# Optimization experiments

Hardware: AMD Instinct MI355X
Metric: run time of the kernel (lower is better)

## Reference

```python
import jax, jax.numpy as jnp
import numpy as np

N_REC_STEPS = 50      # fixed-point iterations for geodesic reconstruction
BN_EPS = 1e-3         # keras BatchNormalization default epsilon


def _dilation2d(x, k):
    # tf.nn.dilation2d, SAME padding: out[p,q] = max_{i,j} x[p+i-1,q+j-1] + k[i,j]
    kk = k[:, :, 0, 0]
    H, W = x.shape[1], x.shape[2]
    xp = jnp.pad(x, ((0, 0), (1, 1), (1, 1), (0, 0)), constant_values=-np.inf)
    vals = [xp[:, i:i + H, j:j + W, :] + kk[i, j] for i in range(3) for j in range(3)]
    return jnp.max(jnp.stack(vals, axis=0), axis=0)


def _erosion2d(x, k):
    # tf.nn.erosion2d (kernel mirrored): out[p,q] = min_{i,j} x[p+i-1,q+j-1] - k[-i,-j]
    kk = k[::-1, ::-1, 0, 0]
    H, W = x.shape[1], x.shape[2]
    xp = jnp.pad(x, ((0, 0), (1, 1), (1, 1), (0, 0)), constant_values=np.inf)
    vals = [xp[:, i:i + H, j:j + W, :] - kk[i, j] for i in range(3) for j in range(3)]
    return jnp.min(jnp.stack(vals, axis=0), axis=0)


def _conv_relu(x, w, b):
    y = jax.lax.conv_general_dilated(x, w, (1, 1), 'VALID',
                                     dimension_numbers=('NHWC', 'HWIO', 'NHWC'))
    return jax.nn.relu(y + b)


def _bn(x, g, b, m, v):
    return g * (x - m) * jax.lax.rsqrt(v + BN_EPS) + b


def _maxpool2(x):
    return jax.lax.reduce_window(x, -np.inf, jax.lax.max,
                                 (1, 2, 2, 1), (1, 2, 2, 1), 'VALID')


def _dilate3_same(x):
    # flat 3x3 structuring element (skimage square(3)) geodesic dilation step
    return jax.lax.reduce_window(x, -np.inf, jax.lax.max,
                                 (1, 3, 3, 1), (1, 1, 1, 1), 'SAME')


def _h_maxima(h, mask):
    # reconstruction-by-dilation of (mask - h) under mask
    marker = mask - h
    def step(m, _):
        m = jnp.minimum(_dilate3_same(m), mask)
        return m, None
    rec, _ = jax.lax.scan(step, marker, None, length=N_REC_STEPS)
    return rec


def setup_inputs() -> dict:
    key = jax.random.key(0)
    ks = jax.random.split(key, 8)
    B, H, W = 32, 256, 256
    inp = {
        'x': jax.random.uniform(ks[0], (B, H, W, 1), dtype=jnp.float32),
        'kernel_open': jnp.zeros((3, 3, 1, 1), jnp.float32),   # flat SE (zero-init)
        'kernel_close': jnp.zeros((3, 3, 1, 1), jnp.float32),
        'conv1_w': 0.1 * jax.random.normal(ks[1], (3, 3, 1, 8), jnp.float32),
        'conv1_b': jnp.zeros((8,), jnp.float32),
        'conv2_w': 0.1 * jax.random.normal(ks[2], (3, 3, 8, 16), jnp.float32),
        'conv2_b': jnp.zeros((16,), jnp.float32),
        'conv3_w': 0.1 * jax.random.normal(ks[3], (3, 3, 16, 32), jnp.float32),
        'conv3_b': jnp.zeros((32,), jnp.float32),
        'conv4_w': 0.1 * jax.random.normal(ks[4], (3, 3, 32, 32), jnp.float32),
        'conv4_b': jnp.zeros((32,), jnp.float32),
        'bn1_g': jnp.ones((8,), jnp.float32), 'bn1_b': jnp.zeros((8,), jnp.float32),
        'bn1_m': jnp.zeros((8,), jnp.float32), 'bn1_v': jnp.ones((8,), jnp.float32),
        'bn2_g': jnp.ones((16,), jnp.float32), 'bn2_b': jnp.zeros((16,), jnp.float32),
        'bn2_m': jnp.zeros((16,), jnp.float32), 'bn2_v': jnp.ones((16,), jnp.float32),
        'bn3_g': jnp.ones((32,), jnp.float32), 'bn3_b': jnp.zeros((32,), jnp.float32),
        'bn3_m': jnp.zeros((32,), jnp.float32), 'bn3_v': jnp.ones((32,), jnp.float32),
        'dense_w': 0.05 * jax.random.uniform(ks[5], (32, 1), dtype=jnp.float32),  # NonNeg
        'dense_b': jnp.zeros((1,), jnp.float32),
    }
    return inp


def reference(x, kernel_open, kernel_close,
              conv1_w, conv1_b, conv2_w, conv2_b, conv3_w, conv3_b, conv4_w, conv4_b,
              bn1_g, bn1_b, bn1_m, bn1_v,
              bn2_g, bn2_b, bn2_m, bn2_v,
              bn3_g, bn3_b, bn3_m, bn3_v,
              dense_w, dense_b):
    # Opening2D then Closing2D (morphological pre-filter)
    xo = _dilation2d(_erosion2d(x, kernel_open), kernel_open)
    xc = _erosion2d(_dilation2d(xo, kernel_close), kernel_close)
    y = _conv_relu(xc, conv1_w, conv1_b)                 # (B,254,254,8)
    y = _bn(y, bn1_g, bn1_b, bn1_m, bn1_v)
    y = _conv_relu(y, conv2_w, conv2_b)                  # (B,252,252,16)
    y = _maxpool2(y)                                     # (B,126,126,16)
    y = _bn(y, bn2_g, bn2_b, bn2_m, bn2_v)
    y = _conv_relu(y, conv3_w, conv3_b)                  # (B,124,124,32)
    y = _bn(y, bn3_g, bn3_b, bn3_m, bn3_v)
    y = _conv_relu(y, conv4_w, conv4_b)                  # (B,122,122,32)
    y = _maxpool2(y)                                     # (B,61,61,32)
    y = jnp.max(y, axis=(1, 2))                          # GlobalMaxPooling2D -> (B,32)
    h = y @ dense_w + dense_b                            # (B,1)
    h = h[:, :, None, None]                              # (B,1,1,1)
    # h-maxima transform: reconstruction by dilation of (xc - h) under xc
    out = _h_maxima(h, xc)                               # (B,256,256,1)
    return (out, h)
```

## Files before the change

kernel.cpp:

```cpp
#include <hip/hip_runtime.h>


#define B_ 32
#define H_ 256
#define W_ 256

__device__ __forceinline__ float4 ld4(const float* p){ return *reinterpret_cast<const float4*>(p); }
__device__ __forceinline__ void st4(float* p, float4 v){ *reinterpret_cast<float4*>(p) = v; }
__device__ __forceinline__ void st4s(float* p, float4 v){ *reinterpret_cast<float4*>(p) = v; }

template<int IS_MAX>
__global__ void morph_k(const float* __restrict__ in, float* __restrict__ out,
                        const float* __restrict__ k9)
{
    int t = blockIdx.x * blockDim.x + threadIdx.x;
    int xq = t & 63; int y = (t >> 6) & 255; int b = t >> 14;
    if (b >= B_) return;
    const float INF = __builtin_inff();
    const float* img = in + (size_t)b * (H_ * W_);
    int x0 = xq * 4;
    float res[4];
    #pragma unroll
    for (int j = 0; j < 4; ++j) res[j] = IS_MAX ? -INF : INF;
    #pragma unroll
    for (int di = -1; di <= 1; ++di) {
        int yy = y + di;
        if (yy < 0 || yy >= H_) continue;
        const float* row = img + yy * W_;
        float w[6];
        w[0] = (x0 > 0) ? row[x0 - 1] : (IS_MAX ? -INF : INF);
        float4 m = ld4(row + x0);
        w[1] = m.x; w[2] = m.y; w[3] = m.z; w[4] = m.w;
        w[5] = (x0 + 4 < W_) ? row[x0 + 4] : (IS_MAX ? -INF : INF);
        #pragma unroll
        for (int dj = -1; dj <= 1; ++dj) {
            float kv = IS_MAX ? k9[(di + 1) * 3 + (dj + 1)]
                              : k9[(1 - di) * 3 + (1 - dj)];
            #pragma unroll
            for (int j = 0; j < 4; ++j) {
                float v = IS_MAX ? (w[j + 1 + dj] + kv) : (w[j + 1 + dj] - kv);
                res[j] = IS_MAX ? fmaxf(res[j], v) : fminf(res[j], v);
            }
        }
    }
    st4(out + (size_t)b * (H_ * W_) + y * W_ + x0,
        make_float4(res[0], res[1], res[2], res[3]));
}

__global__ void conv1_k(const float* __restrict__ xc, float* __restrict__ y1,
                        const float* __restrict__ w, const float* __restrict__ bias,
                        const float* __restrict__ g, const float* __restrict__ bb,
                        const float* __restrict__ mn, const float* __restrict__ vr)
{
    const int S = 254;
    int t = blockIdx.x * blockDim.x + threadIdx.x;
    int total = B_ * S * S;
    if (t >= total) return;
    int x = t % S; int y = (t / S) % S; int b = t / (S * S);
    const float* img = xc + (size_t)b * H_ * W_;
    float acc[8];
    #pragma unroll
    for (int c = 0; c < 8; ++c) acc[c] = bias[c];
    #pragma unroll
    for (int ky = 0; ky < 3; ++ky) {
        #pragma unroll
        for (int kx = 0; kx < 3; ++kx) {
            float iv = img[(y + ky) * W_ + (x + kx)];
            const float* wp = w + (ky * 3 + kx) * 8;
            #pragma unroll
            for (int c = 0; c < 8; ++c) acc[c] = fmaf(iv, wp[c], acc[c]);
        }
    }
    float* op = y1 + (size_t)t * 8;
    #pragma unroll
    for (int c = 0; c < 8; ++c) {
        float z = fmaxf(acc[c], 0.f);
        float s = g[c] / sqrtf(vr[c] + 1.0e-3f);
        op[c] = fmaf(s, z, bb[c] - mn[c] * s);
    }
}

__global__ void conv2_k(const float* __restrict__ y1, float* __restrict__ y2,
                        const float* __restrict__ w, const float* __restrict__ bias,
                        const float* __restrict__ g, const float* __restrict__ bb,
                        const float* __restrict__ mn, const float* __restrict__ vr)
{
    const int P = 126, SIN = 254;
    int t = blockIdx.x * blockDim.x + threadIdx.x;
    int total = B_ * P * P;
    if (t >= total) return;
    int px = t % P; int py = (t / P) % P; int b = t / (P * P);
    const float* imgb = y1 + (size_t)b * SIN * SIN * 8;
    float best[16];
    #pragma unroll
    for (int c = 0; c < 16; ++c) best[c] = 0.f;
    #pragma unroll 1
    for (int pos = 0; pos < 4; ++pos) {
        int oy = 2 * py + (pos >> 1), ox = 2 * px + (pos & 1);
        float acc[16];
        #pragma unroll
        for (int c = 0; c < 16; ++c) acc[c] = bias[c];
        #pragma unroll 1
        for (int tap = 0; tap < 9; ++tap) {
            int ky = tap / 3, kx = tap - ky * 3;
            const float* ip = imgb + ((size_t)(oy + ky) * SIN + (ox + kx)) * 8;
            float4 a = ld4(ip), c4 = ld4(ip + 4);
            float in8[8] = {a.x, a.y, a.z, a.w, c4.x, c4.y, c4.z, c4.w};
            const float* wp = w + tap * 8 * 16;
            #pragma unroll
            for (int ci = 0; ci < 8; ++ci)
                #pragma unroll
                for (int co = 0; co < 16; ++co)
                    acc[co] = fmaf(in8[ci], wp[ci * 16 + co], acc[co]);
        }
        #pragma unroll
        for (int co = 0; co < 16; ++co)
            best[co] = fmaxf(best[co], fmaxf(acc[co], 0.f));
    }
    float* op = y2 + (size_t)t * 16;
    #pragma unroll
    for (int c = 0; c < 16; ++c) {
        float s = g[c] / sqrtf(vr[c] + 1.0e-3f);
        op[c] = fmaf(s, best[c], bb[c] - mn[c] * s);
    }
}

template<int CIN, int CIN_P, int SIN>
__device__ __forceinline__ void conv_tile_compute(
    const float* __restrict__ in_b, const float* __restrict__ w,
    const float* __restrict__ bias, float* lds,
    int ty, int tx, int lty, int ltx, int tid, float acc[32])
{
    const int CINq = CIN / 4;
    const int TOT = 18 * 18 * CINq;
    int y0 = ty * 16, x0 = tx * 16;
    for (int i = tid; i < TOT; i += 256) {
        int pix = i / CINq, q = i - pix * CINq;
        int r = pix / 18, c = pix - r * 18;
        int gy = min(y0 + r, SIN - 1), gx = min(x0 + c, SIN - 1);
        float4 v = ld4(in_b + ((size_t)gy * SIN + gx) * CIN + q * 4);
        st4s(lds + (r * 18 + c) * CIN_P + q * 4, v);
    }
    __syncthreads();
    #pragma unroll
    for (int c = 0; c < 32; ++c) acc[c] = bias[c];
    const float* wt = w;
    #pragma unroll 1
    for (int tap = 0; tap < 9; ++tap) {
        int ky = tap / 3, kx = tap - ky * 3;
        const float* lp = lds + ((lty + ky) * 18 + (ltx + kx)) * CIN_P;
        float v[CIN];
        #pragma unroll
        for (int q = 0; q < CINq; ++q) {
            float4 t4 = *reinterpret_cast<const float4*>(lp + q * 4);
            v[q * 4 + 0] = t4.x; v[q * 4 + 1] = t4.y;
            v[q * 4 + 2] = t4.z; v[q * 4 + 3] = t4.w;
        }
        #pragma unroll
        for (int ci = 0; ci < CIN; ++ci)
            #pragma unroll
            for (int co = 0; co < 32; ++co)
                acc[co] = fmaf(v[ci], wt[ci * 32 + co], acc[co]);
        wt += CIN * 32;
    }
}

__global__ void __launch_bounds__(256) conv3t_k(
    const float* __restrict__ y2, float* __restrict__ y3,
    const float* __restrict__ w, const float* __restrict__ bias,
    const float* __restrict__ g, const float* __restrict__ bb,
    const float* __restrict__ mn, const float* __restrict__ vr)
{
    const int SIN = 126, SOUT = 124;
    __shared__ float lds[18 * 18 * 20];
    int blk = blockIdx.x;
    int b = blk >> 6; int tt = blk & 63; int ty = tt >> 3, tx = tt & 7;
    int tid = threadIdx.x, lty = tid >> 4, ltx = tid & 15;
    float acc[32];
    conv_tile_compute<16, 20, 126>(y2 + (size_t)b * SIN * SIN * 16, w, bias,
                                   lds, ty, tx, lty, ltx, tid, acc);
    int oy = ty * 16 + lty, ox = tx * 16 + ltx;
    if (oy < SOUT && ox < SOUT) {
        float* op = y3 + ((size_t)b * SOUT * SOUT + (size_t)oy * SOUT + ox) * 32;
        #pragma unroll
        for (int c = 0; c < 32; ++c) {
            float z = fmaxf(acc[c], 0.f);
            float s = g[c] / sqrtf(vr[c] + 1.0e-3f);
            op[c] = fmaf(s, z, bb[c] - mn[c] * s);
        }
    }
}

__global__ void __launch_bounds__(256) conv4t_k(
    const float* __restrict__ y3, float* __restrict__ maxbuf,
    const float* __restrict__ w, const float* __restrict__ bias)
{
    const int SIN = 124, SOUT = 122;
    __shared__ float lds[18 * 18 * 36];
    __shared__ float red[4 * 32];
    int blk = blockIdx.x;
    int b = blk >> 6; int tt = blk & 63; int ty = tt >> 3, tx = tt & 7;
    int tid = threadIdx.x, lty = tid >> 4, ltx = tid & 15;
    float acc[32];
    conv_tile_compute<32, 36, 124>(y3 + (size_t)b * SIN * SIN * 32, w, bias,
                                   lds, ty, tx, lty, ltx, tid, acc);
    int oy = ty * 16 + lty, ox = tx * 16 + ltx;
    bool valid = (oy < SOUT) && (ox < SOUT);
    #pragma unroll
    for (int c = 0; c < 32; ++c)
        acc[c] = valid ? fmaxf(acc[c], 0.f) : 0.f;
    int lane = tid & 63, wid = tid >> 6;
    #pragma unroll 1
    for (int c = 0; c < 32; ++c) {
        float v = acc[c];
        #pragma unroll
        for (int off = 32; off >= 1; off >>= 1)
            v = fmaxf(v, __shfl_xor(v, off, 64));
        if (lane == 0) red[wid * 32 + c] = v;
    }
    __syncthreads();
    if (tid < 32) {
        int c = tid;
        float mx = fmaxf(fmaxf(red[0 * 32 + c], red[1 * 32 + c]),
                         fmaxf(red[2 * 32 + c], red[3 * 32 + c]));
        atomicMax(reinterpret_cast<int*>(maxbuf) + b * 32 + c, __float_as_int(mx));
    }
}

__global__ void dense_k(const float* __restrict__ maxbuf, const float* __restrict__ dw,
                        const float* __restrict__ db, float* __restrict__ hbuf,
                        float* __restrict__ out_h)
{
    int t = threadIdx.x;
    if (t < B_) {
        float acc = db[0];
        #pragma unroll
        for (int c = 0; c < 32; ++c) acc = fmaf(maxbuf[t * 32 + c], dw[c], acc);
        hbuf[t] = acc;
        out_h[t] = acc;
    }
}

__global__ void minit_k(const float* __restrict__ xc, const float* __restrict__ hbuf,
                        float* __restrict__ m0)
{
    int t = blockIdx.x * blockDim.x + threadIdx.x;
    int b = t >> 14;
    if (b >= B_) return;
    float hv = hbuf[b];
    float4 a = ld4(xc + (size_t)t * 4);
    st4(m0 + (size_t)t * 4, make_float4(a.x - hv, a.y - hv, a.z - hv, a.w - hv));
}

#define FS_R   5
#define FS_IW  80
#define FS_IH  42
__global__ void __launch_bounds__(256) fstep_k(
    const float* __restrict__ msrc, const float* __restrict__ mask,
    float* __restrict__ mdst)
{
    __shared__ float bufA[FS_IH * FS_IW];
    __shared__ float bufB[FS_IH * FS_IW];
    __shared__ float mk[FS_IH * FS_IW];
    const float NINF = -__builtin_inff();

    int blk = blockIdx.x;
    int img = blk >> 5; int tt = blk & 31; int ty = tt >> 2, tx = tt & 3;
    int gy0 = ty * 32 - FS_R;
    int gx0 = tx * 64 - 8;
    int tid = threadIdx.x;
    const float* src_b = msrc + (size_t)img * (H_ * W_);
    const float* msk_b = mask + (size_t)img * (H_ * W_);

    for (int i = tid; i < FS_IH * FS_IW; i += 256) {
        int r = i / FS_IW, c = i - r * FS_IW;
        int gy = gy0 + r, gx = gx0 + c;
        bool in = (gy >= 0) && (gy < H_) && (gx >= 0) && (gx < W_);
        int gidx = gy * W_ + gx;
        bufA[i] = in ? src_b[gidx] : NINF;
        mk[i]   = in ? msk_b[gidx] : NINF;
    }
    __syncthreads();

    float* cur = bufA;
    float* nxt = bufB;
    #pragma unroll 1
    for (int s = 0; s < FS_R; ++s) {
        for (int i = tid; i < FS_IH * (FS_IW / 4); i += 256) {
            int r = i / (FS_IW / 4), q = i - r * (FS_IW / 4);
            int c = q * 4;
            int rm = (r > 0) ? r - 1 : 0, rp = (r < FS_IH - 1) ? r + 1 : FS_IH - 1;
            float h0, h1, h2, h3;
            {
                const float* rw = cur + rm * FS_IW;
                float4 a = *reinterpret_cast<const float4*>(rw + c);
                float L = rw[(c > 0) ? c - 1 : 0];
                float R = rw[(c + 4 < FS_IW) ? c + 4 : FS_IW - 1];
                h0 = fmaxf(fmaxf(L, a.x), a.y);
                h1 = fmaxf(fmaxf(a.x, a.y), a.z);
                h2 = fmaxf(fmaxf(a.y, a.z), a.w);
                h3 = fmaxf(fmaxf(a.z, a.w), R);
            }
            {
                const float* rw = cur + r * FS_IW;
                float4 a = *reinterpret_cast<const float4*>(rw + c);
                float L = rw[(c > 0) ? c - 1 : 0];
                float R = rw[(c + 4 < FS_IW) ? c + 4 : FS_IW - 1];
                h0 = fmaxf(h0, fmaxf(fmaxf(L, a.x), a.y));
                h1 = fmaxf(h1, fmaxf(fmaxf(a.x, a.y), a.z));
                h2 = fmaxf(h2, fmaxf(fmaxf(a.y, a.z), a.w));
                h3 = fmaxf(h3, fmaxf(fmaxf(a.z, a.w), R));
            }
            {
                const float* rw = cur + rp * FS_IW;
                float4 a = *reinterpret_cast<const float4*>(rw + c);
                float L = rw[(c > 0) ? c - 1 : 0];
                float R = rw[(c + 4 < FS_IW) ? c + 4 : FS_IW - 1];
                h0 = fmaxf(h0, fmaxf(fmaxf(L, a.x), a.y));
                h1 = fmaxf(h1, fmaxf(fmaxf(a.x, a.y), a.z));
                h2 = fmaxf(h2, fmaxf(fmaxf(a.y, a.z), a.w));
                h3 = fmaxf(h3, fmaxf(fmaxf(a.z, a.w), R));
            }
            float4 m4 = *reinterpret_cast<const float4*>(mk + r * FS_IW + c);
            float4 o;
            o.x = fminf(h0, m4.x); o.y = fminf(h1, m4.y);
            o.z = fminf(h2, m4.z); o.w = fminf(h3, m4.w);
            *reinterpret_cast<float4*>(nxt + r * FS_IW + c) = o;
        }
        __syncthreads();
        float* tmp = cur; cur = nxt; nxt = tmp;
    }

    float* dst_b = mdst + (size_t)img * (H_ * W_);
    for (int i = tid; i < 32 * 16; i += 256) {
        int r = i >> 4, q = i & 15;
        float4 v = *reinterpret_cast<const float4*>(cur + (FS_R + r) * FS_IW + 8 + q * 4);
        *reinterpret_cast<float4*>(dst_b + (ty * 32 + r) * W_ + tx * 64 + q * 4) = v;
    }
}

extern "C" void kernel_launch(void* const* d_in, const int* in_sizes, int n_in,
                              void* d_out, int out_size, void* d_ws, size_t ws_size,
                              hipStream_t stream) {
    const float* x    = (const float*)d_in[0];
    const float* ko   = (const float*)d_in[1];
    const float* kc   = (const float*)d_in[2];
    const float* c1w  = (const float*)d_in[3];
    const float* c1b  = (const float*)d_in[4];
    const float* c2w  = (const float*)d_in[5];
    const float* c2b  = (const float*)d_in[6];
    const float* c3w  = (const float*)d_in[7];
    const float* c3b  = (const float*)d_in[8];
    const float* c4w  = (const float*)d_in[9];
    const float* c4b  = (const float*)d_in[10];
    const float* bn1g = (const float*)d_in[11];
    const float* bn1b = (const float*)d_in[12];
    const float* bn1m = (const float*)d_in[13];
    const float* bn1v = (const float*)d_in[14];
    const float* bn2g = (const float*)d_in[15];
    const float* bn2b = (const float*)d_in[16];
    const float* bn2m = (const float*)d_in[17];
    const float* bn2v = (const float*)d_in[18];
    const float* bn3g = (const float*)d_in[19];
    const float* bn3b = (const float*)d_in[20];
    const float* bn3m = (const float*)d_in[21];
    const float* bn3v = (const float*)d_in[22];
    const float* dw   = (const float*)d_in[23];
    const float* db   = (const float*)d_in[24];
    float* out = (float*)d_out;
    float* ws  = (float*)d_ws;

    float* xc     = ws;
    float* A      = ws + 2097152;
    float* Bbuf   = ws + 18613248;
    float* maxbuf = ws + 26741760;
    float* hbuf   = ws + 26742784;
    float* t0 = A;
    float* t1 = A + 2097152;

    const int NQ_BLOCKS = (B_ * H_ * W_ / 4) / 256;

    morph_k<0><<<NQ_BLOCKS, 256, 0, stream>>>(x,  t0, ko);
    morph_k<1><<<NQ_BLOCKS, 256, 0, stream>>>(t0, t1, ko);
    morph_k<1><<<NQ_BLOCKS, 256, 0, stream>>>(t1, t0, kc);
    morph_k<0><<<NQ_BLOCKS, 256, 0, stream>>>(t0, xc, kc);

    conv1_k<<<(B_ * 254 * 254 + 255) / 256, 256, 0, stream>>>(xc, A, c1w, c1b,
                                                              bn1g, bn1b, bn1m, bn1v);
    conv2_k<<<(B_ * 126 * 126 + 255) / 256, 256, 0, stream>>>(A, Bbuf, c2w, c2b,
                                                              bn2g, bn2b, bn2m, bn2v);
    conv3t_k<<<B_ * 64, 256, 0, stream>>>(Bbuf, A, c3w, c3b, bn3g, bn3b, bn3m, bn3v);
    hipMemsetAsync(maxbuf, 0, 32 * 32 * sizeof(float), stream);
    conv4t_k<<<B_ * 64, 256, 0, stream>>>(A, maxbuf, c4w, c4b);
    dense_k<<<1, 64, 0, stream>>>(maxbuf, dw, db, hbuf, out + B_ * H_ * W_);

    minit_k<<<NQ_BLOCKS, 256, 0, stream>>>(xc, hbuf, t0);
    for (int j = 0; j < 10; ++j) {
        const float* src = (j & 1) ? t1 : t0;
        float* dst = (j == 9) ? out : ((j & 1) ? t0 : t1);
        fstep_k<<<B_ * 32, 256, 0, stream>>>(src, xc, dst);
    }
}
```

Measured before the change: 674.0 us.

## Tile conv2 through LDS and chunk conv4 input channels to cut LDS use

Conv2+maxpool becomes a tiled kernel. Each block stages a 34x34x8 input patch in shared memory in channel-planar layout and computes four conv outputs per thread before pooling, replacing uncoalesced per-thread global loads. Conv4 now loads its 32 input channels in two 16-channel chunks, shrinking its shared tile from 36 to 20 floats per pixel so more blocks can be resident per CU. The cost is an extra barrier and reload pass in conv4, and a larger per-thread register accumulator (64 floats) in conv2.

```diff
diff --git a/kernel.cpp b/kernel.cpp
--- a/kernel.cpp
+++ b/kernel.cpp
@@ -80,88 +80,112 @@
     }
 }
 
-__global__ void conv2_k(const float* __restrict__ y1, float* __restrict__ y2,
-                        const float* __restrict__ w, const float* __restrict__ bias,
-                        const float* __restrict__ g, const float* __restrict__ bb,
-                        const float* __restrict__ mn, const float* __restrict__ vr)
-{
-    const int P = 126, SIN = 254;
-    int t = blockIdx.x * blockDim.x + threadIdx.x;
-    int total = B_ * P * P;
-    if (t >= total) return;
-    int px = t % P; int py = (t / P) % P; int b = t / (P * P);
-    const float* imgb = y1 + (size_t)b * SIN * SIN * 8;
-    float best[16];
-    #pragma unroll
-    for (int c = 0; c < 16; ++c) best[c] = 0.f;
+#define C2_PITCH (34 * 34 + 2)
+__global__ void __launch_bounds__(256) conv2t_k(
+    const float* __restrict__ y1, float* __restrict__ y2,
+    const float* __restrict__ w, const float* __restrict__ bias,
+    const float* __restrict__ g, const float* __restrict__ bb,
+    const float* __restrict__ mn, const float* __restrict__ vr)
+{
+    const int SIN = 254, POUT = 126;
+    __shared__ float lds[8 * C2_PITCH];
+    int blk = blockIdx.x;
+    int b = blk >> 6; int tt = blk & 63; int ty = tt >> 3, tx = tt & 7;
+    int cy0 = ty * 32, cx0 = tx * 32;
+    int tid = threadIdx.x;
+    const float* in_b = y1 + (size_t)b * SIN * SIN * 8;
+
+    for (int i = tid; i < 34 * 34; i += 256) {
+        int r = i / 34, c = i - r * 34;
+        int gy = min(cy0 + r, SIN - 1), gx = min(cx0 + c, SIN - 1);
+        const float* p = in_b + ((size_t)gy * SIN + gx) * 8;
+        float4 a = ld4(p), d = ld4(p + 4);
+        lds[0 * C2_PITCH + i] = a.x; lds[1 * C2_PITCH + i] = a.y;
+        lds[2 * C2_PITCH + i] = a.z; lds[3 * C2_PITCH + i] = a.w;
+        lds[4 * C2_PITCH + i] = d.x; lds[5 * C2_PITCH + i] = d.y;
+        lds[6 * C2_PITCH + i] = d.z; lds[7 * C2_PITCH + i] = d.w;
+    }
+    __syncthreads();
+
+    int lty = tid >> 4, ltx = tid & 15;
+    float acc[4][16];
+    #pragma unroll
+    for (int pos = 0; pos < 4; ++pos)
+        #pragma unroll
+        for (int c = 0; c < 16; ++c) acc[pos][c] = bias[c];
+
     #pragma unroll 1
-    for (int pos = 0; pos < 4; ++pos) {
-        int oy = 2 * py + (pos >> 1), ox = 2 * px + (pos & 1);
-        float acc[16];
-        #pragma unroll
-        for (int c = 0; c < 16; ++c) acc[c] = bias[c];
+    for (int tap = 0; tap < 9; ++tap) {
+        int ky = tap / 3, kx = tap - ky * 3;
+        const float* wp = w + tap * 8 * 16;
+        #pragma unroll
+        for (int pos = 0; pos < 4; ++pos) {
+            int pix = (2 * lty + (pos >> 1) + ky) * 34 + (2 * ltx + (pos & 1) + kx);
+            float in8[8];
+            #pragma unroll
+            for (int ci = 0; ci < 8; ++ci) in8[ci] = lds[ci * C2_PITCH + pix];
+            #pragma unroll
+            for (int ci = 0; ci < 8; ++ci)
+                #pragma unroll
+                for (int co = 0; co < 16; ++co)
+                    acc[pos][co] = fmaf(in8[ci], wp[ci * 16 + co], acc[pos][co]);
+        }
+    }
+
+    int py = ty * 16 + lty, px = tx * 16 + ltx;
+    if (py < POUT && px < POUT) {
+        float* op = y2 + ((size_t)b * POUT * POUT + (size_t)py * POUT + px) * 16;
+        #pragma unroll
+        for (int co = 0; co < 16; ++co) {
+            float bst = fmaxf(fmaxf(fmaxf(acc[0][co], 0.f), fmaxf(acc[1][co], 0.f)),
+                              fmaxf(fmaxf(acc[2][co], 0.f), fmaxf(acc[3][co], 0.f)));
+            float s = g[co] / sqrtf(vr[co] + 1.0e-3f);
+            op[co] = fmaf(s, bst, bb[co] - mn[co] * s);
+        }
+    }
+}
+
+template<int CIN, int NCH, int CHP, int SIN>
+__device__ __forceinline__ void conv_tile_chunked(
+    const float* __restrict__ in_b, const float* __restrict__ w,
+    const float* __restrict__ bias, float* lds,
+    int y0, int x0, int lty, int ltx, int tid, float acc[32])
+{
+    const int CHUNK = CIN / NCH, CHQ = CHUNK / 4;
+    #pragma unroll
+    for (int c = 0; c < 32; ++c) acc[c] = bias[c];
+    #pragma unroll 1
+    for (int ch = 0; ch < NCH; ++ch) {
+        int ci0 = ch * CHUNK;
+        if (ch) __syncthreads();
+        const int TOT = 18 * 18 * CHQ;
+        for (int i = tid; i < TOT; i += 256) {
+            int pix = i / CHQ, q = i - pix * CHQ;
+            int r = pix / 18, c = pix - r * 18;
+            int gy = min(y0 + r, SIN - 1), gx = min(x0 + c, SIN - 1);
+            float4 v = ld4(in_b + ((size_t)gy * SIN + gx) * CIN + ci0 + q * 4);
+            st4s(lds + (r * 18 + c) * CHP + q * 4, v);
+        }
+        __syncthreads();
+        const float* wb = w + ci0 * 32;
         #pragma unroll 1
         for (int tap = 0; tap < 9; ++tap) {
             int ky = tap / 3, kx = tap - ky * 3;
-            const float* ip = imgb + ((size_t)(oy + ky) * SIN + (ox + kx)) * 8;
-            float4 a = ld4(ip), c4 = ld4(ip + 4);
-            float in8[8] = {a.x, a.y, a.z, a.w, c4.x, c4.y, c4.z, c4.w};
-            const float* wp = w + tap * 8 * 16;
-            #pragma unroll
-            for (int ci = 0; ci < 8; ++ci)
+            const float* lp = lds + ((lty + ky) * 18 + (ltx + kx)) * CHP;
+            float v[CHUNK];
+            #pragma unroll
+            for (int q = 0; q < CHQ; ++q) {
+                float4 t4 = *reinterpret_cast<const float4*>(lp + q * 4);
+                v[q * 4 + 0] = t4.x; v[q * 4 + 1] = t4.y;
+                v[q * 4 + 2] = t4.z; v[q * 4 + 3] = t4.w;
+            }
+            const float* wt = wb + tap * CIN * 32;
+            #pragma unroll
+            for (int ci = 0; ci < CHUNK; ++ci)
                 #pragma unroll
-                for (int co = 0; co < 16; ++co)
-                    acc[co] = fmaf(in8[ci], wp[ci * 16 + co], acc[co]);
-        }
-        #pragma unroll
-        for (int co = 0; co < 16; ++co)
-            best[co] = fmaxf(best[co], fmaxf(acc[co], 0.f));
-    }
-    float* op = y2 + (size_t)t * 16;
-    #pragma unroll
-    for (int c = 0; c < 16; ++c) {
-        float s = g[c] / sqrtf(vr[c] + 1.0e-3f);
-        op[c] = fmaf(s, best[c], bb[c] - mn[c] * s);
-    }
-}
-
-template<int CIN, int CIN_P, int SIN>
-__device__ __forceinline__ void conv_tile_compute(
-    const float* __restrict__ in_b, const float* __restrict__ w,
-    const float* __restrict__ bias, float* lds,
-    int ty, int tx, int lty, int ltx, int tid, float acc[32])
-{
-    const int CINq = CIN / 4;
-    const int TOT = 18 * 18 * CINq;
-    int y0 = ty * 16, x0 = tx * 16;
-    for (int i = tid; i < TOT; i += 256) {
-        int pix = i / CINq, q = i - pix * CINq;
-        int r = pix / 18, c = pix - r * 18;
-        int gy = min(y0 + r, SIN - 1), gx = min(x0 + c, SIN - 1);
-        float4 v = ld4(in_b + ((size_t)gy * SIN + gx) * CIN + q * 4);
-        st4s(lds + (r * 18 + c) * CIN_P + q * 4, v);
-    }
-    __syncthreads();
-    #pragma unroll
-    for (int c = 0; c < 32; ++c) acc[c] = bias[c];
-    const float* wt = w;
-    #pragma unroll 1
-    for (int tap = 0; tap < 9; ++tap) {
-        int ky = tap / 3, kx = tap - ky * 3;
-        const float* lp = lds + ((lty + ky) * 18 + (ltx + kx)) * CIN_P;
-        float v[CIN];
-        #pragma unroll
-        for (int q = 0; q < CINq; ++q) {
-            float4 t4 = *reinterpret_cast<const float4*>(lp + q * 4);
-            v[q * 4 + 0] = t4.x; v[q * 4 + 1] = t4.y;
-            v[q * 4 + 2] = t4.z; v[q * 4 + 3] = t4.w;
-        }
-        #pragma unroll
-        for (int ci = 0; ci < CIN; ++ci)
-            #pragma unroll
-            for (int co = 0; co < 32; ++co)
-                acc[co] = fmaf(v[ci], wt[ci * 32 + co], acc[co]);
-        wt += CIN * 32;
+                for (int co = 0; co < 32; ++co)
+                    acc[co] = fmaf(v[ci], wt[ci * 32 + co], acc[co]);
+        }
     }
 }
 
@@ -177,8 +201,8 @@
     int b = blk >> 6; int tt = blk & 63; int ty = tt >> 3, tx = tt & 7;
     int tid = threadIdx.x, lty = tid >> 4, ltx = tid & 15;
     float acc[32];
-    conv_tile_compute<16, 20, 126>(y2 + (size_t)b * SIN * SIN * 16, w, bias,
-                                   lds, ty, tx, lty, ltx, tid, acc);
+    conv_tile_chunked<16, 1, 20, 126>(y2 + (size_t)b * SIN * SIN * 16, w, bias,
+                                      lds, ty * 16, tx * 16, lty, ltx, tid, acc);
     int oy = ty * 16 + lty, ox = tx * 16 + ltx;
     if (oy < SOUT && ox < SOUT) {
         float* op = y3 + ((size_t)b * SOUT * SOUT + (size_t)oy * SOUT + ox) * 32;
@@ -196,14 +220,14 @@
     const float* __restrict__ w, const float* __restrict__ bias)
 {
     const int SIN = 124, SOUT = 122;
-    __shared__ float lds[18 * 18 * 36];
+    __shared__ float lds[18 * 18 * 20];
     __shared__ float red[4 * 32];
     int blk = blockIdx.x;
     int b = blk >> 6; int tt = blk & 63; int ty = tt >> 3, tx = tt & 7;
     int tid = threadIdx.x, lty = tid >> 4, ltx = tid & 15;
     float acc[32];
-    conv_tile_compute<32, 36, 124>(y3 + (size_t)b * SIN * SIN * 32, w, bias,
-                                   lds, ty, tx, lty, ltx, tid, acc);
+    conv_tile_chunked<32, 2, 20, 124>(y3 + (size_t)b * SIN * SIN * 32, w, bias,
+                                      lds, ty * 16, tx * 16, lty, ltx, tid, acc);
     int oy = ty * 16 + lty, ox = tx * 16 + ltx;
     bool valid = (oy < SOUT) && (ox < SOUT);
     #pragma unroll
@@ -387,8 +411,7 @@
 
     conv1_k<<<(B_ * 254 * 254 + 255) / 256, 256, 0, stream>>>(xc, A, c1w, c1b,
                                                               bn1g, bn1b, bn1m, bn1v);
-    conv2_k<<<(B_ * 126 * 126 + 255) / 256, 256, 0, stream>>>(A, Bbuf, c2w, c2b,
-                                                              bn2g, bn2b, bn2m, bn2v);
+    conv2t_k<<<B_ * 64, 256, 0, stream>>>(A, Bbuf, c2w, c2b, bn2g, bn2b, bn2m, bn2v);
     conv3t_k<<<B_ * 64, 256, 0, stream>>>(Bbuf, A, c3w, c3b, bn3g, bn3b, bn3m, bn3v);
     hipMemsetAsync(maxbuf, 0, 32 * 32 * sizeof(float), stream);
     conv4t_k<<<B_ * 64, 256, 0, stream>>>(A, maxbuf, c4w, c4b);
```

Result: faster. 573.6 us (-14.9%).
